# Optimization experiments

Hardware: AMD Instinct MI355X
Metric: run time of the kernel (lower is better)

The kernel has to match this reference:

```python
import jax, jax.numpy as jnp
import numpy as np

NEG_SLOPE = 0.2  # PyG GATv2Conv default leaky_relu negative slope


def _gatv2_layer(x, src, dst, n, Wl, bl, Wr, br, att, bias, concat):
    # PyG GATv2Conv (share_weights=False, edge_dim=None):
    #   x_l = lin_l(x) on source, x_r = lin_r(x) on target
    #   m = leaky_relu(x_l[src] + x_r[dst]); alpha = softmax_dst(<m, att>)
    #   out[i] = sum_{e: dst=i} alpha_e * x_l[src_e]
    H, C = att.shape
    xl = (x @ Wl + bl).reshape(n, H, C)
    xr = (x @ Wr + br).reshape(n, H, C)
    m = jax.nn.leaky_relu(xl[src] + xr[dst], NEG_SLOPE)      # [E,H,C]
    logits = jnp.einsum('ehc,hc->eh', m, att)                # [E,H]
    lmax = jax.ops.segment_max(logits, dst, num_segments=n)  # [N,H]
    e = jnp.exp(logits - lmax[dst])
    denom = jax.ops.segment_sum(e, dst, num_segments=n)
    alpha = e / (denom[dst] + 1e-16)                         # [E,H]
    out = jax.ops.segment_sum(xl[src] * alpha[:, :, None], dst, num_segments=n)
    out = out.reshape(n, H * C) if concat else out.mean(axis=1)
    return out + bias


def _glorot(key, shape):
    fan_in, fan_out = shape[0], shape[-1]
    s = jnp.sqrt(6.0 / (fan_in + fan_out))
    return jax.random.uniform(key, shape, jnp.float32, -s, s)


def setup_inputs() -> dict:
    key = jax.random.key(0)
    N, E, B = 50000, 800000, 512
    node_in, hidden, heads, meta_dim = 128, 32, 4, 12
    ks = jax.random.split(key, 32)
    inp = {
        'x': jax.random.normal(ks[0], (N, node_in), jnp.float32),
        'edge_index': jax.random.randint(ks[1], (2, E), 0, N, jnp.int64),
        'batch': jnp.sort(jax.random.randint(ks[2], (N,), 0, B, jnp.int64)),
        'metadata': jax.random.normal(ks[3], (B, meta_dim), jnp.float32),
    }
    dims = [(node_in, hidden, heads), (hidden * heads, hidden, heads), (hidden * heads, hidden, 1)]
    i = 4
    for li, (din, dh, H) in enumerate(dims):
        inp[f'Wl{li}'] = _glorot(ks[i], (din, H * dh)); i += 1
        inp[f'bl{li}'] = jnp.zeros((H * dh,), jnp.float32)
        inp[f'Wr{li}'] = _glorot(ks[i], (din, H * dh)); i += 1
        inp[f'br{li}'] = jnp.zeros((H * dh,), jnp.float32)
        inp[f'att{li}'] = _glorot(ks[i], (H, dh)); i += 1
        out_dim = H * dh if li < 2 else dh  # last layer concat=False
        inp[f'b{li}'] = jnp.zeros((out_dim,), jnp.float32)
    pool_dim = hidden  # n_layers=3 -> final single-head layer
    inp['Wh1'] = _glorot(ks[i], (pool_dim + meta_dim, pool_dim)); i += 1
    inp['bh1'] = jnp.zeros((pool_dim,), jnp.float32)
    inp['Wh2'] = _glorot(ks[i], (pool_dim, 1)); i += 1
    inp['bh2'] = jnp.zeros((1,), jnp.float32)
    return inp


def reference(x, edge_index, batch, metadata,
              Wl0, bl0, Wr0, br0, att0, b0,
              Wl1, bl1, Wr1, br1, att1, b1,
              Wl2, bl2, Wr2, br2, att2, b2,
              Wh1, bh1, Wh2, bh2):
    n = x.shape[0]
    B = metadata.shape[0]
    # PyG GATv2Conv add_self_loops=True
    loop = jnp.arange(n, dtype=edge_index.dtype)
    src = jnp.concatenate([edge_index[0], loop])
    dst = jnp.concatenate([edge_index[1], loop])
    params = [(Wl0, bl0, Wr0, br0, att0, b0, True),
              (Wl1, bl1, Wr1, br1, att1, b1, True),
              (Wl2, bl2, Wr2, br2, att2, b2, False)]
    h = x
    for (Wl, bl, Wr, br, att, bias, concat) in params:
        h = _gatv2_layer(h, src, dst, n, Wl, bl, Wr, br, att, bias, concat)
        h = jax.nn.elu(h)  # dropout is identity in eval mode
    # global mean pool over graphs
    sums = jax.ops.segment_sum(h, batch, num_segments=B)
    cnt = jax.ops.segment_sum(jnp.ones((n,), h.dtype), batch, num_segments=B)
    emb = sums / jnp.clip(cnt, 1.0)[:, None]
    z = jnp.concatenate([emb, metadata], axis=1)
    z = jax.nn.relu(z @ Wh1 + bh1)
    return z @ Wh2 + bh2  # (B, 1) logits
```

## Files before the change

kernel.cpp:

```cpp
#include <hip/hip_runtime.h>
#include <cstdint>
#include <cstddef>

#define NEG_SLOPE 0.2f
#define LOG2E 1.44269504f

typedef __attribute__((ext_vector_type(8))) short short8;
typedef __attribute__((ext_vector_type(4))) float f32x4;

__device__ __forceinline__ float bf2f(unsigned short u) {
    union { unsigned int i; float f; } x; x.i = ((unsigned int)u) << 16; return x.f;
}
__device__ __forceinline__ unsigned short f2bf(float f) {
    union { float f; unsigned int i; } x;
    x.f = f;
    unsigned int u = x.i;
    return (unsigned short)((u + 0x7FFFu + ((u >> 16) & 1u)) >> 16);
}

__device__ __forceinline__ float dpp_sum8(float p) {
    p += __int_as_float(__builtin_amdgcn_update_dpp(0, __float_as_int(p), 0xB1, 0xF, 0xF, true));
    p += __int_as_float(__builtin_amdgcn_update_dpp(0, __float_as_int(p), 0x4E, 0xF, 0xF, true));
    p += __int_as_float(__builtin_amdgcn_update_dpp(0, __float_as_int(p), 0x141, 0xF, 0xF, true));
    return p;
}

__global__ __launch_bounds__(256) void prep_w_all(
    const float* __restrict__ Wl0, const float* __restrict__ Wr0,
    const float* __restrict__ Wl1, const float* __restrict__ Wr1,
    const float* __restrict__ Wl2, const float* __restrict__ Wr2,
    unsigned short* __restrict__ Bt0, unsigned short* __restrict__ Bt1,
    unsigned short* __restrict__ Bt2, int* __restrict__ cnt, int N)
{
    int idx = blockIdx.x * 256 + threadIdx.x;
    for (int i = idx; i < N; i += gridDim.x * 256) cnt[i] = 0;
    const int SZ = 256 * 128;
    const float *Wl, *Wr; unsigned short* Bt; int dout;
    if (idx < SZ)              { Wl = Wl0; Wr = Wr0; Bt = Bt0; dout = 128; }
    else if (idx < 2 * SZ)     { Wl = Wl1; Wr = Wr1; Bt = Bt1; dout = 128; idx -= SZ; }
    else if (idx < 2 * SZ + 64 * 128) { Wl = Wl2; Wr = Wr2; Bt = Bt2; dout = 32; idx -= 2 * SZ; }
    else return;
    int n = idx >> 7, k = idx & 127;
    float v = (n < dout) ? Wl[(size_t)k * dout + n] : Wr[(size_t)k * dout + (n - dout)];
    Bt[idx] = f2bf(v);
}

template<int BN, bool ABF16>
__global__ __launch_bounds__(256) void gemm_mfma(
    const void* __restrict__ Avoid, int M,
    const unsigned short* __restrict__ Bt,
    const float* __restrict__ bl, const float* __restrict__ br,
    int dout, unsigned short* __restrict__ XL, unsigned short* __restrict__ XR)
{
    constexpr int LDA = 136;
    constexpr int NT  = BN / 16;
    __shared__ __attribute__((aligned(16))) unsigned short Bs[BN * LDA];
    const int t  = threadIdx.x;
    const int m0 = blockIdx.x * 64;
    const int n0 = blockIdx.y * BN;

    const int w    = t >> 6;
    const int lane = t & 63;
    const int fr   = lane & 15;
    const int quad = lane >> 4;

#pragma unroll
    for (int i = 0; i < BN / 16; ++i) {
        int c  = t + i * 256;
        int n  = c >> 4;
        int kc = (c & 15) * 8;
        *(short8*)(Bs + n * LDA + kc) =
            *(const short8*)(Bt + (size_t)(n0 + n) * 128 + kc);
    }

    const int arow = m0 + w * 16 + fr;
    const size_t abase = (size_t)(arow < M ? arow : 0) * 128 + quad * 8;
    short8 afr[4];
    if (ABF16) {
        const unsigned short* A = (const unsigned short*)Avoid;
#pragma unroll
        for (int kk = 0; kk < 4; ++kk)
            afr[kk] = *(const short8*)(A + abase + kk * 32);
    } else {
        const float* A = (const float*)Avoid;
#pragma unroll
        for (int kk = 0; kk < 4; ++kk) {
            float4 lo = *(const float4*)(A + abase + kk * 32);
            float4 hi = *(const float4*)(A + abase + kk * 32 + 4);
            afr[kk][0] = (short)f2bf(lo.x); afr[kk][1] = (short)f2bf(lo.y);
            afr[kk][2] = (short)f2bf(lo.z); afr[kk][3] = (short)f2bf(lo.w);
            afr[kk][4] = (short)f2bf(hi.x); afr[kk][5] = (short)f2bf(hi.y);
            afr[kk][6] = (short)f2bf(hi.z); afr[kk][7] = (short)f2bf(hi.w);
        }
    }
    __syncthreads();

    f32x4 acc[NT] = {};
    const unsigned short* bp = Bs + fr * LDA + quad * 8;
#pragma unroll
    for (int kk = 0; kk < 4; ++kk) {
#pragma unroll
        for (int j = 0; j < NT; ++j) {
            short8 bfr = *(const short8*)(bp + j * 16 * LDA + kk * 32);
            acc[j] = __builtin_amdgcn_mfma_f32_16x16x32_bf16(afr[kk], bfr, acc[j], 0, 0, 0);
        }
    }

#pragma unroll
    for (int j = 0; j < NT; ++j) {
        int col = n0 + j * 16 + fr;
        float bias = (col < dout) ? bl[col] : br[col - dout];
#pragma unroll
        for (int r = 0; r < 4; ++r) {
            int row = m0 + w * 16 + quad * 4 + r;
            if (row < M) {
                unsigned short o = f2bf(acc[j][r] + bias);
                if (col < dout) XL[(size_t)row * dout + col] = o;
                else            XR[(size_t)row * dout + (col - dout)] = o;
            }
        }
    }
}

__global__ void count_rank_kernel(const int* __restrict__ dst, int E,
                                  int* __restrict__ cnt, unsigned short* __restrict__ rank)
{
    int e = blockIdx.x * blockDim.x + threadIdx.x;
    if (e < E) {
        int p = atomicAdd(&cnt[dst[e]], 1);
        rank[e] = (unsigned short)p;
    }
}

__global__ __launch_bounds__(256) void scan_partial(
    const int* __restrict__ cnt, int N, int* __restrict__ bsum)
{
    __shared__ int red[4];
    const int t = threadIdx.x;
    const int base = blockIdx.x * 2048;
    int s = 0;
#pragma unroll
    for (int i = 0; i < 8; ++i) {
        int idx = base + t + i * 256;
        if (idx < N) s += cnt[idx];
    }
#pragma unroll
    for (int off = 32; off >= 1; off >>= 1) s += __shfl_xor(s, off);
    if ((t & 63) == 0) red[t >> 6] = s;
    __syncthreads();
    if (t == 0) bsum[blockIdx.x] = red[0] + red[1] + red[2] + red[3];
}

__global__ __launch_bounds__(256) void scan_bsums(
    int* __restrict__ bsum, int nb, int E, int* __restrict__ rowptr, int N)
{
    __shared__ int sh[256];
    const int t = threadIdx.x;
    int v = (t < nb) ? bsum[t] : 0;
    sh[t] = v;
    __syncthreads();
    for (int off = 1; off < 256; off <<= 1) {
        int u = (t >= off) ? sh[t - off] : 0;
        __syncthreads();
        sh[t] += u;
        __syncthreads();
    }
    if (t < nb) bsum[t] = sh[t] - v;
    if (t == 0) rowptr[N] = E;
}

__global__ __launch_bounds__(256) void scan_final(
    const int* __restrict__ cnt, int N, const int* __restrict__ bsum,
    int* __restrict__ rowptr)
{
    __shared__ int sdat[2048];
    __shared__ int tsum[256];
    const int t = threadIdx.x;
    const int base = blockIdx.x * 2048;
#pragma unroll
    for (int i = 0; i < 8; ++i) {
        int idx = base + t + i * 256;
        sdat[t + i * 256] = (idx < N) ? cnt[idx] : 0;
    }
    __syncthreads();
    int vals[8];
    int s = 0;
#pragma unroll
    for (int j = 0; j < 8; ++j) { vals[j] = sdat[t * 8 + j]; s += vals[j]; }
    tsum[t] = s;
    __syncthreads();
    for (int off = 1; off < 256; off <<= 1) {
        int u = (t >= off) ? tsum[t - off] : 0;
        __syncthreads();
        tsum[t] += u;
        __syncthreads();
    }
    int run = bsum[blockIdx.x] + tsum[t] - s;
#pragma unroll
    for (int j = 0; j < 8; ++j) { sdat[t * 8 + j] = run; run += vals[j]; }
    __syncthreads();
#pragma unroll
    for (int i = 0; i < 8; ++i) {
        int idx = base + t + i * 256;
        if (idx < N) rowptr[idx] = sdat[t + i * 256];
    }
}

__global__ void place_kernel(const int* __restrict__ src, const int* __restrict__ dst,
                             const unsigned short* __restrict__ rank, int E,
                             const int* __restrict__ rowptr,
                             unsigned short* __restrict__ csr_src)
{
    int e = blockIdx.x * blockDim.x + threadIdx.x;
    if (e < E)
        csr_src[rowptr[dst[e]] + rank[e]] = (unsigned short)src[e];
}

template<int H>
__global__ __launch_bounds__(256, 4) void gat_fused(
    const unsigned short* __restrict__ xl, const unsigned short* __restrict__ xr,
    const int* __restrict__ rowptr, const unsigned short* __restrict__ csr_src,
    const float* __restrict__ att, const float* __restrict__ bias,
    unsigned short* __restrict__ hout, int hstride, int N)
{
    constexpr int HC  = 32 * H;
    constexpr int LPE = HC / 4;
    constexpr int EPW = 64 / LPE;
    const int node = blockIdx.x * 4 + (threadIdx.x >> 6);
    if (node >= N) return;
    const int lane = threadIdx.x & 63;
    const int q    = lane % LPE;
    const int slot = lane / LPE;
    const int rs   = rowptr[node];
    const int re   = rowptr[node + 1];

    const unsigned short* __restrict__ xlb = xl + 4 * q;
    float4 xri;
    {
        ushort4 u = *(const ushort4*)(xr + (size_t)node * HC + 4 * q);
        xri.x = bf2f(u.x); xri.y = bf2f(u.y); xri.z = bf2f(u.z); xri.w = bf2f(u.w);
    }
    float4 b1, b2;
    {
        float4 a = *(const float4*)(att + 4 * q);
        const float c1 = 0.5f * (1.0f + NEG_SLOPE) * LOG2E;
        const float c2 = 0.5f * (1.0f - NEG_SLOPE) * LOG2E;
        b1.x = a.x * c1; b1.y = a.y * c1; b1.z = a.z * c1; b1.w = a.w * c1;
        b2.x = a.x * c2; b2.y = a.y * c2; b2.z = a.z * c2; b2.w = a.w * c2;
    }

    float l = 0.f;
    float4 acc = make_float4(0.f, 0.f, 0.f, 0.f);

    auto ld4 = [&](int s) -> float4 {
        ushort4 u = *(const ushort4*)(xlb + (size_t)s * HC);
        float4 v;
        v.x = bf2f(u.x); v.y = bf2f(u.y); v.z = bf2f(u.z); v.w = bf2f(u.w);
        return v;
    };

    auto edge_w = [&](const float4& v) -> float {
        float sx = v.x + xri.x, sy = v.y + xri.y, sz = v.z + xri.z, sw = v.w + xri.w;
        float p  = b1.x * sx;
        float pq = b2.x * fabsf(sx);
        p  = fmaf(b1.y, sy, p);
        pq = fmaf(b2.y, fabsf(sy), pq);
        p  = fmaf(b1.z, sz, p);
        pq = fmaf(b2.z, fabsf(sz), pq);
        p  = fmaf(b1.w, sw, p);
        pq = fmaf(b2.w, fabsf(sw), pq);
        p += pq;
        p = dpp_sum8(p);
        return exp2f(p);
    };

    if (slot == 0) {
        float4 v = ld4(node);
        float w = edge_w(v);
        l = w;
        acc.x = w * v.x; acc.y = w * v.y; acc.z = w * v.z; acc.w = w * v.w;
    }

    int k = rs + slot;
    for (; k + EPW < re; k += 2 * EPW) {
        int s0 = csr_src[k];
        int s1 = csr_src[k + EPW];
        float4 v0 = ld4(s0);
        float4 v1 = ld4(s1);
        float w0 = edge_w(v0);
        float w1 = edge_w(v1);
        l += w0 + w1;
        acc.x = fmaf(w0, v0.x, fmaf(w1, v1.x, acc.x));
        acc.y = fmaf(w0, v0.y, fmaf(w1, v1.y, acc.y));
        acc.z = fmaf(w0, v0.z, fmaf(w1, v1.z, acc.z));
        acc.w = fmaf(w0, v0.w, fmaf(w1, v1.w, acc.w));
    }
    if (k < re) {
        int s0 = csr_src[k];
        float4 v0 = ld4(s0);
        float w0 = edge_w(v0);
        l += w0;
        acc.x = fmaf(w0, v0.x, acc.x);
        acc.y = fmaf(w0, v0.y, acc.y);
        acc.z = fmaf(w0, v0.z, acc.z);
        acc.w = fmaf(w0, v0.w, acc.w);
    }

#pragma unroll
    for (int mask = LPE; mask < 64; mask <<= 1) {
        l     += __shfl_xor(l, mask);
        acc.x += __shfl_xor(acc.x, mask);
        acc.y += __shfl_xor(acc.y, mask);
        acc.z += __shfl_xor(acc.z, mask);
        acc.w += __shfl_xor(acc.w, mask);
    }

    if (lane < LPE) {
        const float4 bi = *(const float4*)(bias + 4 * q);
        float inv = 1.f / (l + 1e-16f);
        float4 o;
        o.x = acc.x * inv + bi.x;
        o.y = acc.y * inv + bi.y;
        o.z = acc.z * inv + bi.z;
        o.w = acc.w * inv + bi.w;
        o.x = (o.x > 0.f) ? o.x : expm1f(o.x);
        o.y = (o.y > 0.f) ? o.y : expm1f(o.y);
        o.z = (o.z > 0.f) ? o.z : expm1f(o.z);
        o.w = (o.w > 0.f) ? o.w : expm1f(o.w);
        ushort4 ob;
        ob.x = f2bf(o.x); ob.y = f2bf(o.y); ob.z = f2bf(o.z); ob.w = f2bf(o.w);
        *(ushort4*)(hout + (size_t)node * hstride + 4 * q) = ob;
    }
}

__global__ __launch_bounds__(128) void pool_head_kernel(
    const unsigned short* __restrict__ h, int hstride,
    const int* __restrict__ batch, int N,
    const float* __restrict__ meta,
    const float* __restrict__ Wh1, const float* __restrict__ bh1,
    const float* __restrict__ Wh2, const float* __restrict__ bh2,
    float* __restrict__ out)
{
    const int b = blockIdx.x;
    const int t = threadIdx.x;
    __shared__ float s[128];
    __shared__ float z[44];

    int lo = 0, hi = N;
    while (lo < hi) { int mid = (lo + hi) >> 1; if (batch[mid] < b) lo = mid + 1; else hi = mid; }
    int lo2 = lo, hi2 = N;
    while (lo2 < hi2) { int mid = (lo2 + hi2) >> 1; if (batch[mid] < b + 1) lo2 = mid + 1; else hi2 = mid; }
    const int start = lo, end = lo2;

    const int c = t & 31, r = t >> 5;
    float acc = 0.f;
    for (int row = start + r; row < end; row += 4)
        acc += bf2f(h[(size_t)row * hstride + c]);
    s[t] = acc;
    __syncthreads();
    if (t < 32) {
        float sum = s[t] + s[t + 32] + s[t + 64] + s[t + 96];
        z[t] = sum / fmaxf((float)(end - start), 1.0f);
    } else if (t < 44) {
        z[t] = meta[(size_t)b * 12 + (t - 32)];
    }
    __syncthreads();
    if (t < 32) {
        float hj = bh1[t];
#pragma unroll
        for (int k = 0; k < 44; ++k)
            hj = fmaf(z[k], Wh1[k * 32 + t], hj);
        hj = fmaxf(hj, 0.f);
        float p = hj * Wh2[t];
#pragma unroll
        for (int off = 16; off >= 1; off >>= 1)
            p += __shfl_xor(p, off, 32);
        if (t == 0) out[b] = p + bh2[0];
    }
}

extern "C" void kernel_launch(void* const* d_in, const int* in_sizes, int n_in,
                              void* d_out, int out_size, void* d_ws, size_t ws_size,
                              hipStream_t stream)
{
    const float* x     = (const float*)d_in[0];
    const int*   ei    = (const int*)d_in[1];
    const int*   batch = (const int*)d_in[2];
    const float* meta  = (const float*)d_in[3];
    const float* Wl[3]  = {(const float*)d_in[4],  (const float*)d_in[10], (const float*)d_in[16]};
    const float* bl[3]  = {(const float*)d_in[5],  (const float*)d_in[11], (const float*)d_in[17]};
    const float* Wr[3]  = {(const float*)d_in[6],  (const float*)d_in[12], (const float*)d_in[18]};
    const float* br[3]  = {(const float*)d_in[7],  (const float*)d_in[13], (const float*)d_in[19]};
    const float* att[3] = {(const float*)d_in[8],  (const float*)d_in[14], (const float*)d_in[20]};
    const float* bb[3]  = {(const float*)d_in[9],  (const float*)d_in[15], (const float*)d_in[21]};
    const float* Wh1 = (const float*)d_in[22];
    const float* bh1 = (const float*)d_in[23];
    const float* Wh2 = (const float*)d_in[24];
    const float* bh2 = (const float*)d_in[25];
    float* out = (float*)d_out;

    const int N  = in_sizes[0] / 128;
    const int E  = in_sizes[1] / 2;
    const int B  = in_sizes[3] / 12;
    const int NB = (N + 2047) / 2048;

    char* wsp = (char*)d_ws;
    size_t off_ = 0;
    auto alloc = [&](size_t bytes) {
        char* p = wsp + off_;
        off_ = (off_ + bytes + 255) & ~(size_t)255;
        return p;
    };
    unsigned short* xlbuf = (unsigned short*)alloc((size_t)N * 128 * 2);
    unsigned short* xrbuf = (unsigned short*)alloc((size_t)N * 128 * 2);
    unsigned short* hbuf  = (unsigned short*)alloc((size_t)N * 128 * 2);
    int*   cnt     = (int*)alloc((size_t)N * 4);
    int*   rowptr  = (int*)alloc((size_t)(N + 1) * 4);
    unsigned short* rank    = (unsigned short*)alloc((size_t)E * 2);
    unsigned short* csr_src = (unsigned short*)alloc((size_t)E * 2);
    unsigned short* Bt0     = (unsigned short*)alloc((size_t)256 * 128 * 2);
    unsigned short* Bt1     = (unsigned short*)alloc((size_t)256 * 128 * 2);
    unsigned short* Bt2     = (unsigned short*)alloc((size_t)64 * 128 * 2);
    int*   bsum    = (int*)alloc((size_t)256 * 4);

    const int* srcI = ei;
    const int* dstI = ei + E;

    prep_w_all<<<(2 * 256 * 128 + 64 * 128 + 255) / 256, 256, 0, stream>>>(
        Wl[0], Wr[0], Wl[1], Wr[1], Wl[2], Wr[2], Bt0, Bt1, Bt2, cnt, N);

    count_rank_kernel<<<(E + 255) / 256, 256, 0, stream>>>(dstI, E, cnt, rank);
    scan_partial<<<NB, 256, 0, stream>>>(cnt, N, bsum);
    scan_bsums<<<1, 256, 0, stream>>>(bsum, NB, E, rowptr, N);
    scan_final<<<NB, 256, 0, stream>>>(cnt, N, bsum, rowptr);
    place_kernel<<<(E + 255) / 256, 256, 0, stream>>>(srcI, dstI, rank, E, rowptr, csr_src);

    const int GB = (N + 3) / 4;
    const int MB = (N + 63) / 64;

    {
        gemm_mfma<128, false><<<dim3(MB, 2), 256, 0, stream>>>(x, N, Bt0, bl[0], br[0], 128, xlbuf, xrbuf);
        gat_fused<4><<<GB, 256, 0, stream>>>(xlbuf, xrbuf, rowptr, csr_src, att[0], bb[0], hbuf, 128, N);
    }
    {
        gemm_mfma<128, true><<<dim3(MB, 2), 256, 0, stream>>>(hbuf, N, Bt1, bl[1], br[1], 128, xlbuf, xrbuf);
        gat_fused<4><<<GB, 256, 0, stream>>>(xlbuf, xrbuf, rowptr, csr_src, att[1], bb[1], hbuf, 128, N);
    }
    {
        gemm_mfma<64, true><<<dim3(MB, 1), 256, 0, stream>>>(hbuf, N, Bt2, bl[2], br[2], 32, xlbuf, xrbuf);
        gat_fused<1><<<GB, 256, 0, stream>>>(xlbuf, xrbuf, rowptr, csr_src, att[2], bb[2], hbuf, 32, N);
    }
    pool_head_kernel<<<B, 128, 0, stream>>>(hbuf, 32, batch, N, meta, Wh1, bh1, Wh2, bh2, out);
}
```

Before: 361.0 us.

## Replace global-atomic CSR build with two-level radix bucket sort

```diff
diff --git a/kernel.cpp b/kernel.cpp
--- a/kernel.cpp
+++ b/kernel.cpp
@@ -4,6 +4,7 @@
 
 #define NEG_SLOPE 0.2f
 #define LOG2E 1.44269504f
+#define NBLK 256
 
 typedef __attribute__((ext_vector_type(8))) short short8;
 typedef __attribute__((ext_vector_type(4))) float f32x4;
@@ -30,10 +31,9 @@
     const float* __restrict__ Wl1, const float* __restrict__ Wr1,
     const float* __restrict__ Wl2, const float* __restrict__ Wr2,
     unsigned short* __restrict__ Bt0, unsigned short* __restrict__ Bt1,
-    unsigned short* __restrict__ Bt2, int* __restrict__ cnt, int N)
+    unsigned short* __restrict__ Bt2)
 {
     int idx = blockIdx.x * 256 + threadIdx.x;
-    for (int i = idx; i < N; i += gridDim.x * 256) cnt[i] = 0;
     const int SZ = 256 * 128;
     const float *Wl, *Wr; unsigned short* Bt; int dout;
     if (idx < SZ)              { Wl = Wl0; Wr = Wr0; Bt = Bt0; dout = 128; }
@@ -122,13 +122,71 @@
     }
 }
 
-__global__ void count_rank_kernel(const int* __restrict__ dst, int E,
-                                  int* __restrict__ cnt, unsigned short* __restrict__ rank)
-{
-    int e = blockIdx.x * blockDim.x + threadIdx.x;
-    if (e < E) {
-        int p = atomicAdd(&cnt[dst[e]], 1);
-        rank[e] = (unsigned short)p;
+__global__ __launch_bounds__(256) void csr_hist(
+    const int* __restrict__ dst, int E, int tile, int* __restrict__ hist)
+{
+    __shared__ int h[256];
+    const int t = threadIdx.x, b = blockIdx.x;
+    h[t] = 0;
+    __syncthreads();
+    const int e0 = b * tile;
+    const int e1 = min(E, e0 + tile);
+    for (int e = e0 + t; e < e1; e += 256)
+        atomicAdd(&h[dst[e] >> 8], 1);
+    __syncthreads();
+    hist[t * NBLK + b] = h[t];
+}
+
+__global__ __launch_bounds__(256) void csr_scatter(
+    const int* __restrict__ src, const int* __restrict__ dst, int E, int tile,
+    const int* __restrict__ hist_s, unsigned int* __restrict__ sorted)
+{
+    __shared__ int cur[256];
+    const int t = threadIdx.x, b = blockIdx.x;
+    cur[t] = hist_s[t * NBLK + b];
+    __syncthreads();
+    const int e0 = b * tile;
+    const int e1 = min(E, e0 + tile);
+    for (int e = e0 + t; e < e1; e += 256) {
+        int d = dst[e];
+        int pos = atomicAdd(&cur[d >> 8], 1);
+        sorted[pos] = ((unsigned int)d << 16) | (unsigned int)src[e];
+    }
+}
+
+__global__ __launch_bounds__(256) void csr_fine(
+    const unsigned int* __restrict__ sorted, int E, int N,
+    const int* __restrict__ hist_s,
+    int* __restrict__ rowptr, unsigned short* __restrict__ csr_src)
+{
+    __shared__ int h[256];
+    __shared__ int sc[256];
+    const int t = threadIdx.x, d = blockIdx.x;
+    const int start = hist_s[d * NBLK];
+    const int end   = (d < 255) ? hist_s[(d + 1) * NBLK] : E;
+    h[t] = 0;
+    __syncthreads();
+    for (int e = start + t; e < end; e += 256)
+        atomicAdd(&h[(sorted[e] >> 16) & 0xFF], 1);
+    __syncthreads();
+    int v = h[t];
+    sc[t] = v;
+    __syncthreads();
+    for (int off = 1; off < 256; off <<= 1) {
+        int u = (t >= off) ? sc[t - off] : 0;
+        __syncthreads();
+        sc[t] += u;
+        __syncthreads();
+    }
+    const int base = start + sc[t] - v;
+    const int node = (d << 8) + t;
+    if (node <= N) rowptr[node] = base;
+    h[t] = base;
+    __syncthreads();
+    for (int e = start + t; e < end; e += 256) {
+        unsigned int it = sorted[e];
+        int pos = atomicAdd(&h[(it >> 16) & 0xFF], 1);
+        csr_src[pos] = (unsigned short)(it & 0xFFFFu);
     }
 }
 
@@ -204,16 +262,6 @@
         int idx = base + t + i * 256;
         if (idx < N) rowptr[idx] = sdat[t + i * 256];
     }
-}
-
-__global__ void place_kernel(const int* __restrict__ src, const int* __restrict__ dst,
-                             const unsigned short* __restrict__ rank, int E,
-                             const int* __restrict__ rowptr,
-                             unsigned short* __restrict__ csr_src)
-{
-    int e = blockIdx.x * blockDim.x + threadIdx.x;
-    if (e < E)
-        csr_src[rowptr[dst[e]] + rank[e]] = (unsigned short)src[e];
 }
 
 template<int H>
@@ -402,7 +450,6 @@
     const int N  = in_sizes[0] / 128;
     const int E  = in_sizes[1] / 2;
     const int B  = in_sizes[3] / 12;
-    const int NB = (N + 2047) / 2048;
 
     char* wsp = (char*)d_ws;
     size_t off_ = 0;
@@ -414,10 +461,11 @@
     unsigned short* xlbuf = (unsigned short*)alloc((size_t)N * 128 * 2);
     unsigned short* xrbuf = (unsigned short*)alloc((size_t)N * 128 * 2);
     unsigned short* hbuf  = (unsigned short*)alloc((size_t)N * 128 * 2);
-    int*   cnt     = (int*)alloc((size_t)N * 4);
     int*   rowptr  = (int*)alloc((size_t)(N + 1) * 4);
-    unsigned short* rank    = (unsigned short*)alloc((size_t)E * 2);
     unsigned short* csr_src = (unsigned short*)alloc((size_t)E * 2);
+    unsigned int*   sorted  = (unsigned int*)alloc((size_t)E * 4);
+    int*   hist_g  = (int*)alloc((size_t)65536 * 4);
+    int*   hist_s  = (int*)alloc((size_t)65537 * 4);
     unsigned short* Bt0     = (unsigned short*)alloc((size_t)256 * 128 * 2);
     unsigned short* Bt1     = (unsigned short*)alloc((size_t)256 * 128 * 2);
     unsigned short* Bt2     = (unsigned short*)alloc((size_t)64 * 128 * 2);
@@ -427,13 +475,15 @@
     const int* dstI = ei + E;
 
     prep_w_all<<<(2 * 256 * 128 + 64 * 128 + 255) / 256, 256, 0, stream>>>(
-        Wl[0], Wr[0], Wl[1], Wr[1], Wl[2], Wr[2], Bt0, Bt1, Bt2, cnt, N);
-
-    count_rank_kernel<<<(E + 255) / 256, 256, 0, stream>>>(dstI, E, cnt, rank);
-    scan_partial<<<NB, 256, 0, stream>>>(cnt, N, bsum);
-    scan_bsums<<<1, 256, 0, stream>>>(bsum, NB, E, rowptr, N);
-    scan_final<<<NB, 256, 0, stream>>>(cnt, N, bsum, rowptr);
-    place_kernel<<<(E + 255) / 256, 256, 0, stream>>>(srcI, dstI, rank, E, rowptr, csr_src);
+        Wl[0], Wr[0], Wl[1], Wr[1], Wl[2], Wr[2], Bt0, Bt1, Bt2);
+
+    const int tile = (E + NBLK - 1) / NBLK;
+    csr_hist<<<NBLK, 256, 0, stream>>>(dstI, E, tile, hist_g);
+    scan_partial<<<32, 256, 0, stream>>>(hist_g, 65536, bsum);
+    scan_bsums<<<1, 256, 0, stream>>>(bsum, 32, E, hist_s, 65536);
+    scan_final<<<32, 256, 0, stream>>>(hist_g, 65536, bsum, hist_s);
+    csr_scatter<<<NBLK, 256, 0, stream>>>(srcI, dstI, E, tile, hist_s, sorted);
+    csr_fine<<<(N >> 8) + 1, 256, 0, stream>>>(sorted, E, N, hist_s, rowptr, csr_src);
 
     const int GB = (N + 3) / 4;
     const int MB = (N + 63) / 64;
```

After: 340.8 us. 5.6% less time.
